# Kernel tuning notes

Hardware: AMD Instinct MI355X
Metric: run time of the kernel (lower is better)

The kernel has to match this reference:

```python
import jax, jax.numpy as jnp
import numpy as np

D_MODEL, D_INNER, D_STATE, D_CONV, DT_RANK = 192, 384, 16, 4, 12
EPS = 1e-5


def _causal_dwconv(x, w, b):
    # x: (B, L, Din); w: (Din, 1, K) depthwise; causal left pad K-1
    xc = x.transpose(0, 2, 1)  # (B, Din, L)
    y = jax.lax.conv_general_dilated(xc, w, window_strides=(1,),
                                     padding=[(D_CONV - 1, 0)],
                                     feature_group_count=D_INNER,
                                     dimension_numbers=('NCH', 'OIH', 'NCH'))
    return (y + b[None, :, None]).transpose(0, 2, 1)  # (B, L, Din)


def _ssm_dir(xh, z, conv_w, conv_b, x_proj_w, dt_w, dt_b, A_log, D):
    # one direction of the selective scan
    x = jax.nn.silu(_causal_dwconv(xh, conv_w, conv_b))  # (B, L, Din)
    x_dbl = jnp.einsum('bld,ed->ble', x, x_proj_w)       # (B, L, R+2N)
    dt = jax.nn.softplus(jnp.einsum('blr,dr->bld', x_dbl[..., :DT_RANK], dt_w) + dt_b)
    Bm = x_dbl[..., DT_RANK:DT_RANK + D_STATE]           # (B, L, N)
    Cm = x_dbl[..., DT_RANK + D_STATE:]                  # (B, L, N)
    A = -jnp.exp(A_log)                                  # (Din, N)
    deltaA = jnp.exp(dt[..., None] * A)                  # (B, L, Din, N)
    dBx = (dt * x)[..., None] * Bm[:, :, None, :]        # (B, L, Din, N)

    def comb(e1, e2):
        a1, b1 = e1
        a2, b2 = e2
        return a1 * a2, a2 * b1 + b2

    _, h = jax.lax.associative_scan(comb, (deltaA, dBx), axis=1)
    y = jnp.einsum('bldn,bln->bld', h, Cm) + x * D
    return y * jax.nn.silu(z)


def setup_inputs() -> dict:
    key = jax.random.key(0)
    ks = jax.random.split(key, 24)
    B, L = 2, 2048
    s = 0.02
    inp = {
        'hidden_states': jax.random.normal(ks[0], (B, L, D_MODEL), jnp.float32),
        'residual': jax.random.normal(ks[1], (B, L, D_MODEL), jnp.float32),
        'norm_w': jnp.ones((D_MODEL,), jnp.float32),
        'in_proj_w': jax.random.normal(ks[2], (2 * D_INNER, D_MODEL)) * s,
        'out_proj_w': jax.random.normal(ks[3], (D_MODEL, D_INNER)) * s,
        # forward-direction SSM params
        'conv_w_f': jax.random.normal(ks[4], (D_INNER, 1, D_CONV)) * s,
        'conv_b_f': jnp.zeros((D_INNER,), jnp.float32),
        'x_proj_w_f': jax.random.normal(ks[5], (DT_RANK + 2 * D_STATE, D_INNER)) * s,
        'dt_w_f': jax.random.normal(ks[6], (D_INNER, DT_RANK)) * s,
        'dt_b_f': jax.random.uniform(ks[7], (D_INNER,), minval=-4.0, maxval=-2.0),
        'A_log_f': jnp.log(jnp.tile(jnp.arange(1, D_STATE + 1, dtype=jnp.float32), (D_INNER, 1))),
        'D_f': jnp.ones((D_INNER,), jnp.float32),
        # backward-direction SSM params (bimamba)
        'conv_w_b': jax.random.normal(ks[8], (D_INNER, 1, D_CONV)) * s,
        'conv_b_b': jnp.zeros((D_INNER,), jnp.float32),
        'x_proj_w_b': jax.random.normal(ks[9], (DT_RANK + 2 * D_STATE, D_INNER)) * s,
        'dt_w_b': jax.random.normal(ks[10], (D_INNER, DT_RANK)) * s,
        'dt_b_b': jax.random.uniform(ks[11], (D_INNER,), minval=-4.0, maxval=-2.0),
        'A_log_b': jnp.log(jnp.tile(jnp.arange(1, D_STATE + 1, dtype=jnp.float32), (D_INNER, 1))),
        'D_b': jnp.ones((D_INNER,), jnp.float32),
    }
    return inp


def reference(hidden_states, residual, norm_w, in_proj_w, out_proj_w,
              conv_w_f, conv_b_f, x_proj_w_f, dt_w_f, dt_b_f, A_log_f, D_f,
              conv_w_b, conv_b_b, x_proj_w_b, dt_w_b, dt_b_b, A_log_b, D_b):
    # fused add + RMSNorm (prenorm=True): residual_out = hidden + residual (fp32)
    residual_out = (hidden_states + residual).astype(jnp.float32)
    x = residual_out * jax.lax.rsqrt(jnp.mean(residual_out * residual_out, axis=-1, keepdims=True) + EPS)
    x = x * norm_w
    # Mamba mixer, bimamba=True
    xz = jnp.einsum('bld,ed->ble', x, in_proj_w)  # (B, L, 2*Din)
    xh, z = xz[..., :D_INNER], xz[..., D_INNER:]
    y_f = _ssm_dir(xh, z, conv_w_f, conv_b_f, x_proj_w_f, dt_w_f, dt_b_f, A_log_f, D_f)
    y_b = _ssm_dir(xh[:, ::-1], z[:, ::-1], conv_w_b, conv_b_b, x_proj_w_b, dt_w_b, dt_b_b, A_log_b, D_b)[:, ::-1]
    out = jnp.einsum('bld,ed->ble', y_f + y_b, out_proj_w)
    return out, residual_out
```

## Files before the change

### kernel.cpp

```cpp
#include <hip/hip_runtime.h>
#include <math.h>

#define BB 2
#define LL 2048
#define DM 192
#define DI 384
#define DS 16
#define RK 12
#define NROW (BB*LL)
#define NCH 64
#define CLEN (LL/NCH)

typedef __attribute__((ext_vector_type(8))) short bf16x8;
typedef __attribute__((ext_vector_type(4))) float f32x4;

__device__ __forceinline__ float siluf(float v) { return v / (1.f + __expf(-v)); }

__device__ __forceinline__ unsigned short f2bf(float f) {
  unsigned int x = __float_as_uint(f);
  unsigned int r = (x + 0x7fffu + ((x >> 16) & 1u)) >> 16;
  return (unsigned short)r;
}
__device__ __forceinline__ float bf2f(unsigned short u) {
  return __uint_as_float(((unsigned int)u) << 16);
}

#define N_BFIN  (6*48*512)
#define N_BFOUT (12*12*512)
#define N_BFXP  (2*12*4*512)
#define N_DT    (2*RK*DI)
#define N_PREP  (N_BFIN + N_BFOUT + N_BFXP + N_DT)

__global__ __launch_bounds__(256) void k_wprep(
    const float* __restrict__ wip, const float* __restrict__ wop,
    const float* __restrict__ xpwf, const float* __restrict__ xpwb,
    const float* __restrict__ dtwf, const float* __restrict__ dtwb,
    unsigned short* __restrict__ bin, unsigned short* __restrict__ bout,
    unsigned short* __restrict__ bxp, float* __restrict__ wdt) {
  int i = blockIdx.x * 256 + threadIdx.x;
  if (i < N_BFIN) {
    int j = i & 7, l = (i >> 3) & 63, ng = (i >> 9) % 48, ks = i / (48 * 512);
    int k = ks * 32 + (l >> 4) * 8 + j, c = ng * 16 + (l & 15);
    bin[i] = f2bf(wip[c * DM + k]);
  } else if (i < N_BFIN + N_BFOUT) {
    int t = i - N_BFIN;
    int j = t & 7, l = (t >> 3) & 63, ng = (t >> 9) % 12, ks = t / (12 * 512);
    int k = ks * 32 + (l >> 4) * 8 + j, c = ng * 16 + (l & 15);
    bout[t] = f2bf(wop[c * DI + k]);
  } else if (i < N_BFIN + N_BFOUT + N_BFXP) {
    int t = i - N_BFIN - N_BFOUT;
    int j = t & 7, l = (t >> 3) & 63, ng = (t >> 9) & 3, ks = (t >> 11) % 12;
    int dir = t / (12 * 4 * 512);
    int k = ks * 32 + (l >> 4) * 8 + j, e = ng * 16 + (l & 15);
    const float* src = dir ? xpwb : xpwf;
    bxp[t] = (e < RK + 2 * DS) ? f2bf(src[e * DI + k]) : (unsigned short)0;
  } else if (i < N_PREP) {
    int t = i - N_BFIN - N_BFOUT - N_BFXP;
    int dir = t / (RK * DI), rem = t % (RK * DI);
    int j = rem / DI, d = rem % DI;
    const float* src = dir ? dtwb : dtwf;
    wdt[t] = src[d * RK + j];
  }
}

__global__ __launch_bounds__(256) void k_rmsnorm(
    const float* __restrict__ h, const float* __restrict__ r,
    const float* __restrict__ w, float* __restrict__ res,
    unsigned short* __restrict__ xnb) {
  int row = blockIdx.x * 4 + (threadIdx.x >> 6);
  int lane = threadIdx.x & 63;
  const float* hp = h + row * DM;
  const float* rp = r + row * DM;
  float v0 = hp[lane]       + rp[lane];
  float v1 = hp[lane + 64]  + rp[lane + 64];
  float v2 = hp[lane + 128] + rp[lane + 128];
  float ss = v0 * v0 + v1 * v1 + v2 * v2;
  #pragma unroll
  for (int o = 32; o; o >>= 1) ss += __shfl_xor(ss, o);
  float inv = rsqrtf(ss * (1.f / DM) + 1e-5f);
  float* rr = res + row * DM;
  unsigned short* xo = xnb + row * DM;
  rr[lane] = v0; rr[lane + 64] = v1; rr[lane + 128] = v2;
  xo[lane]       = f2bf(v0 * inv * w[lane]);
  xo[lane + 64]  = f2bf(v1 * inv * w[lane + 64]);
  xo[lane + 128] = f2bf(v2 * inv * w[lane + 128]);
}

__global__ __launch_bounds__(64) void k_inproj(
    const unsigned short* __restrict__ xnb, const unsigned short* __restrict__ bin,
    unsigned short* __restrict__ xhb, unsigned short* __restrict__ zb) {
  int l = threadIdx.x;
  int row0 = blockIdx.x * 16;
  int ng0 = blockIdx.y * 4;
  const unsigned short* arow = xnb + (size_t)(row0 + (l & 15)) * DM + ((l >> 4) * 8);
  f32x4 acc[4];
  #pragma unroll
  for (int g = 0; g < 4; g++) acc[g] = (f32x4){0.f, 0.f, 0.f, 0.f};
  #pragma unroll
  for (int ks = 0; ks < 6; ks++) {
    bf16x8 a = *reinterpret_cast<const bf16x8*>(arow + ks * 32);
    #pragma unroll
    for (int g = 0; g < 4; g++) {
      bf16x8 b = *reinterpret_cast<const bf16x8*>(bin + ((size_t)(ks * 48 + ng0 + g) * 64 + l) * 8);
      acc[g] = __builtin_amdgcn_mfma_f32_16x16x32_bf16(a, b, acc[g], 0, 0, 0);
    }
  }
  int rbase = row0 + (l >> 4) * 4;
  #pragma unroll
  for (int g = 0; g < 4; g++) {
    int col = (ng0 + g) * 16 + (l & 15);
    unsigned short* dst = (col < DI) ? (xhb + col) : (zb + (col - DI));
    #pragma unroll
    for (int r = 0; r < 4; r++) dst[(size_t)(rbase + r) * DI] = f2bf(acc[g][r]);
  }
}

__global__ __launch_bounds__(256) void k_conv(
    const unsigned short* __restrict__ xhb,
    const float* __restrict__ cwf, const float* __restrict__ cbf,
    const float* __restrict__ cwb, const float* __restrict__ cbb,
    unsigned short* __restrict__ xcb) {
  int dir = blockIdx.y;
  int g = blockIdx.x * 256 + threadIdx.x;
  int row = g / DI, d = g % DI;
  int b = row >> 11, s = row & (LL - 1);
  const float* cw = dir ? cwb : cwf;
  const float* cb = dir ? cbb : cbf;
  float acc = cb[d];
  #pragma unroll
  for (int k = 0; k < 4; k++) {
    int sp = s - 3 + k;
    if (sp >= 0) {
      int mr = b * LL + (dir ? (LL - 1 - sp) : sp);
      acc += cw[d * 4 + k] * bf2f(xhb[(size_t)mr * DI + d]);
    }
  }
  xcb[(size_t)(dir * NROW + row) * DI + d] = f2bf(siluf(acc));
}

__global__ __launch_bounds__(128) void k_xpmm(
    const unsigned short* __restrict__ xcb, const unsigned short* __restrict__ bxp,
    const float* __restrict__ wdt_all,
    const float* __restrict__ dtbf, const float* __restrict__ dtbb,
    float* __restrict__ dt, float* __restrict__ Bm, float* __restrict__ Cm) {
  __shared__ float xd[16][48];
  int l = threadIdx.x & 63, w = threadIdx.x >> 6;
  int dir = blockIdx.y;
  int row0 = blockIdx.x * 16;
  const unsigned short* arow = xcb + (size_t)(dir * NROW + row0 + (l & 15)) * DI + ((l >> 4) * 8);
  const unsigned short* wb = bxp + (size_t)dir * 12 * 4 * 512;
  f32x4 acc[2];
  acc[0] = (f32x4){0.f, 0.f, 0.f, 0.f};
  acc[1] = (f32x4){0.f, 0.f, 0.f, 0.f};
  #pragma unroll
  for (int ks = 0; ks < 12; ks++) {
    bf16x8 a = *reinterpret_cast<const bf16x8*>(arow + ks * 32);
    #pragma unroll
    for (int g = 0; g < 2; g++) {
      int ng = w * 2 + g;
      bf16x8 b = *reinterpret_cast<const bf16x8*>(wb + ((size_t)(ks * 4 + ng) * 64 + l) * 8);
      acc[g] = __builtin_amdgcn_mfma_f32_16x16x32_bf16(a, b, acc[g], 0, 0, 0);
    }
  }
  int rbase = (l >> 4) * 4;
  #pragma unroll
  for (int g = 0; g < 2; g++) {
    int col = (w * 2 + g) * 16 + (l & 15);
    #pragma unroll
    for (int r = 0; r < 4; r++) xd[rbase + r][col] = acc[g][r];
  }
  __syncthreads();
  const float* wdt = wdt_all + dir * RK * DI;
  const float* dtb = dir ? dtbb : dtbf;
  int t = threadIdx.x;
  #pragma unroll
  for (int i = 0; i < 48; i++) {
    int idx = i * 128 + t;
    int row = idx / DI, d = idx % DI;
    float a = dtb[d];
    #pragma unroll
    for (int j = 0; j < RK; j++) a = __fmaf_rn(xd[row][j], wdt[j * DI + d], a);
    a = (a > 20.f) ? a : log1pf(__expf(a));
    dt[(size_t)(dir * NROW + row0 + row) * DI + d] = a;
  }
  #pragma unroll
  for (int i = 0; i < 4; i++) {
    int idx = i * 128 + t;
    int row = idx / 32, j = idx % 32;
    float v = xd[row][RK + j];
    if (j < DS) Bm[(size_t)(dir * NROW + row0 + row) * DS + j] = v;
    else        Cm[(size_t)(dir * NROW + row0 + row) * DS + (j - DS)] = v;
  }
}

__global__ __launch_bounds__(128) void k_scan1(
    const float* __restrict__ dt, const unsigned short* __restrict__ xcb,
    const float* __restrict__ Bm,
    const float* __restrict__ Alf, const float* __restrict__ Alb,
    float* __restrict__ S, float* __restrict__ P) {
  int zb = blockIdx.z;
  int dir = zb >> 1;
  int d = blockIdx.x * 128 + threadIdx.x;
  int c = blockIdx.y;
  const float* Al = dir ? Alb : Alf;
  float Av[DS];
  {
    const float4* ap = reinterpret_cast<const float4*>(Al + d * DS);
    #pragma unroll
    for (int q = 0; q < 4; q++) {
      float4 a = ap[q];
      Av[4*q+0] = -__expf(a.x); Av[4*q+1] = -__expf(a.y);
      Av[4*q+2] = -__expf(a.z); Av[4*q+3] = -__expf(a.w);
    }
  }
  int rowbase = zb * LL + c * CLEN;
  const float4* Bp4 = reinterpret_cast<const float4*>(Bm + (size_t)rowbase * DS);
  float h[DS];
  #pragma unroll
  for (int n = 0; n < DS; n++) h[n] = 0.f;
  float sdt = 0.f;
  float dtv = dt[(size_t)rowbase * DI + d];
  float xv  = bf2f(xcb[(size_t)rowbase * DI + d]);
  #pragma unroll 4
  for (int s = 0; s < CLEN; s++) {
    float dtn_ = 0.f, xn_ = 0.f;
    if (s + 1 < CLEN) {
      dtn_ = dt[(size_t)(rowbase + s + 1) * DI + d];
      xn_  = bf2f(xcb[(size_t)(rowbase + s + 1) * DI + d]);
    }
    float4 B0 = Bp4[s*4+0], B1 = Bp4[s*4+1], B2 = Bp4[s*4+2], B3 = Bp4[s*4+3];
    float Bv[DS] = {B0.x,B0.y,B0.z,B0.w, B1.x,B1.y,B1.z,B1.w,
                    B2.x,B2.y,B2.z,B2.w, B3.x,B3.y,B3.z,B3.w};
    float dtx = dtv * xv;
    sdt += dtv;
    #pragma unroll
    for (int n = 0; n < DS; n++) {
      float dA = __expf(dtv * Av[n]);
      h[n] = __fmaf_rn(dA, h[n], dtx * Bv[n]);
    }
    dtv = dtn_; xv = xn_;
  }
  size_t base = ((size_t)(zb * NCH + c) * DI + d) * DS;
  float4* Sp = reinterpret_cast<float4*>(S + base);
  float4* Pp = reinterpret_cast<float4*>(P + base);
  #pragma unroll
  for (int q = 0; q < 4; q++) {
    Sp[q] = make_float4(h[4*q+0], h[4*q+1], h[4*q+2], h[4*q+3]);
    Pp[q] = make_float4(__expf(Av[4*q+0]*sdt), __expf(Av[4*q+1]*sdt),
                        __expf(Av[4*q+2]*sdt), __expf(Av[4*q+3]*sdt));
  }
}

__global__ __launch_bounds__(256) void k_scan2(
    float* __restrict__ S, const float* __restrict__ P) {
  int g = blockIdx.x * 256 + threadIdx.x;
  int zb = g / (DI * DS);
  int rem = g % (DI * DS);
  const int stride = DI * DS;
  size_t base = (size_t)zb * NCH * stride + rem;
  float carry = 0.f;
  for (int c0 = 0; c0 < NCH; c0 += 8) {
    float p8[8], s8[8];
    #pragma unroll
    for (int j = 0; j < 8; j++) {
      p8[j] = P[base + (size_t)(c0 + j) * stride];
      s8[j] = S[base + (size_t)(c0 + j) * stride];
    }
    #pragma unroll
    for (int j = 0; j < 8; j++) {
      S[base + (size_t)(c0 + j) * stride] = carry;
      carry = __fmaf_rn(p8[j], carry, s8[j]);
    }
  }
}

__global__ __launch_bounds__(128) void k_scan3(
    const float* __restrict__ dt, const unsigned short* __restrict__ xcb,
    const float* __restrict__ Bm, const float* __restrict__ Cm,
    const unsigned short* __restrict__ zb_, const float* __restrict__ Hin,
    const float* __restrict__ Alf, const float* __restrict__ Alb,
    const float* __restrict__ Df, const float* __restrict__ Db,
    unsigned short* __restrict__ yb) {
  int zbi = blockIdx.z;
  int dir = zbi >> 1, b = zbi & 1;
  int d = blockIdx.x * 128 + threadIdx.x;
  int c = blockIdx.y;
  const float* Al = dir ? Alb : Alf;
  const float* Dp = dir ? Db : Df;
  float Av[DS];
  {
    const float4* ap = reinterpret_cast<const float4*>(Al + d * DS);
    #pragma unroll
    for (int q = 0; q < 4; q++) {
      float4 a = ap[q];
      Av[4*q+0] = -__expf(a.x); Av[4*q+1] = -__expf(a.y);
      Av[4*q+2] = -__expf(a.z); Av[4*q+3] = -__expf(a.w);
    }
  }
  float Dv = Dp[d];
  int rowbase = zbi * LL + c * CLEN;
  const float4* Bp4 = reinterpret_cast<const float4*>(Bm + (size_t)rowbase * DS);
  const float4* Cp4 = reinterpret_cast<const float4*>(Cm + (size_t)rowbase * DS);
  size_t base = ((size_t)(zbi * NCH + c) * DI + d) * DS;
  float h[DS];
  {
    const float4* hp = reinterpret_cast<const float4*>(Hin + base);
    #pragma unroll
    for (int q = 0; q < 4; q++) {
      float4 a = hp[q];
      h[4*q+0] = a.x; h[4*q+1] = a.y; h[4*q+2] = a.z; h[4*q+3] = a.w;
    }
  }
  float dtv = dt[(size_t)rowbase * DI + d];
  float xv  = bf2f(xcb[(size_t)rowbase * DI + d]);
  #pragma unroll 4
  for (int s = 0; s < CLEN; s++) {
    float dtn_ = 0.f, xn_ = 0.f;
    if (s + 1 < CLEN) {
      dtn_ = dt[(size_t)(rowbase + s + 1) * DI + d];
      xn_  = bf2f(xcb[(size_t)(rowbase + s + 1) * DI + d]);
    }
    float4 B0 = Bp4[s*4+0], B1 = Bp4[s*4+1], B2 = Bp4[s*4+2], B3 = Bp4[s*4+3];
    float Bv[DS] = {B0.x,B0.y,B0.z,B0.w, B1.x,B1.y,B1.z,B1.w,
                    B2.x,B2.y,B2.z,B2.w, B3.x,B3.y,B3.z,B3.w};
    float4 C0 = Cp4[s*4+0], C1 = Cp4[s*4+1], C2 = Cp4[s*4+2], C3 = Cp4[s*4+3];
    float Cv[DS] = {C0.x,C0.y,C0.z,C0.w, C1.x,C1.y,C1.z,C1.w,
                    C2.x,C2.y,C2.z,C2.w, C3.x,C3.y,C3.z,C3.w};
    float dtx = dtv * xv;
    float acc = xv * Dv;
    #pragma unroll
    for (int n = 0; n < DS; n++) {
      float dA = __expf(dtv * Av[n]);
      h[n] = __fmaf_rn(dA, h[n], dtx * Bv[n]);
      acc = __fmaf_rn(h[n], Cv[n], acc);
    }
    int sg = c * CLEN + s;
    int mr = b * LL + (dir ? (LL - 1 - sg) : sg);
    float zv = bf2f(zb_[(size_t)mr * DI + d]);
    yb[(size_t)(rowbase + s) * DI + d] = f2bf(acc * siluf(zv));
    dtv = dtn_; xv = xn_;
  }
}

__global__ __launch_bounds__(64) void k_outproj(
    const unsigned short* __restrict__ yb, const unsigned short* __restrict__ bout,
    float* __restrict__ out) {
  int l = threadIdx.x;
  int row0 = blockIdx.x * 16;
  int ng0 = blockIdx.y * 2;
  int row = row0 + (l & 15);
  int b = row >> 11, ll = row & (LL - 1);
  const unsigned short* yf = yb + (size_t)(b * LL + ll) * DI + (l >> 4) * 8;
  const unsigned short* yr = yb + (size_t)((2 + b) * LL + (LL - 1 - ll)) * DI + (l >> 4) * 8;
  f32x4 acc[2];
  acc[0] = (f32x4){0.f, 0.f, 0.f, 0.f};
  acc[1] = (f32x4){0.f, 0.f, 0.f, 0.f};
  #pragma unroll
  for (int ks = 0; ks < 12; ks++) {
    bf16x8 f8 = *reinterpret_cast<const bf16x8*>(yf + ks * 32);
    bf16x8 g8 = *reinterpret_cast<const bf16x8*>(yr + ks * 32);
    bf16x8 a;
    #pragma unroll
    for (int j = 0; j < 8; j++)
      a[j] = (short)f2bf(bf2f((unsigned short)f8[j]) + bf2f((unsigned short)g8[j]));
    #pragma unroll
    for (int g = 0; g < 2; g++) {
      bf16x8 bb = *reinterpret_cast<const bf16x8*>(bout + ((size_t)(ks * 12 + ng0 + g) * 64 + l) * 8);
      acc[g] = __builtin_amdgcn_mfma_f32_16x16x32_bf16(a, bb, acc[g], 0, 0, 0);
    }
  }
  int rbase = row0 + (l >> 4) * 4;
  #pragma unroll
  for (int g = 0; g < 2; g++) {
    int col = (ng0 + g) * 16 + (l & 15);
    #pragma unroll
    for (int r = 0; r < 4; r++) out[(size_t)(rbase + r) * DM + col] = acc[g][r];
  }
}

extern "C" void kernel_launch(void* const* d_in, const int* in_sizes, int n_in,
                              void* d_out, int out_size, void* d_ws, size_t ws_size,
                              hipStream_t stream) {
  const float* hid  = (const float*)d_in[0];
  const float* res  = (const float*)d_in[1];
  const float* nw   = (const float*)d_in[2];
  const float* wip  = (const float*)d_in[3];
  const float* wop  = (const float*)d_in[4];
  const float* cwf  = (const float*)d_in[5];
  const float* cbf  = (const float*)d_in[6];
  const float* xpwf = (const float*)d_in[7];
  const float* dtwf = (const float*)d_in[8];
  const float* dtbf = (const float*)d_in[9];
  const float* Alf  = (const float*)d_in[10];
  const float* Df   = (const float*)d_in[11];
  const float* cwb  = (const float*)d_in[12];
  const float* cbb  = (const float*)d_in[13];
  const float* xpwb = (const float*)d_in[14];
  const float* dtwb = (const float*)d_in[15];
  const float* dtbb = (const float*)d_in[16];
  const float* Alb  = (const float*)d_in[17];
  const float* Db   = (const float*)d_in[18];

  float* out_p  = (float*)d_out;
  float* resid  = out_p + NROW * DM;

  float* ws = (float*)d_ws;
  float* dt   = ws;
  float* Bm   = dt   + 2 * NROW * DI;
  float* Cm   = Bm   + 2 * NROW * DS;
  float* S    = Cm   + 2 * NROW * DS;
  float* P    = S    + 2 * BB * NCH * DI * DS;
  float* wdt  = P    + 2 * BB * NCH * DI * DS;
  unsigned short* xnb = (unsigned short*)(wdt + N_DT);
  unsigned short* xhb = xnb + NROW * DM;
  unsigned short* zb  = xhb + NROW * DI;
  unsigned short* xcb = zb  + NROW * DI;
  unsigned short* yb  = xcb + 2 * NROW * DI;
  unsigned short* bin = yb  + 2 * NROW * DI;
  unsigned short* bout = bin + N_BFIN;
  unsigned short* bxp  = bout + N_BFOUT;

  k_wprep<<<(N_PREP + 255) / 256, 256, 0, stream>>>(wip, wop, xpwf, xpwb, dtwf, dtwb,
                                                    bin, bout, bxp, wdt);
  k_rmsnorm<<<NROW / 4, 256, 0, stream>>>(hid, res, nw, resid, xnb);
  k_inproj<<<dim3(NROW / 16, 12), 64, 0, stream>>>(xnb, bin, xhb, zb);
  k_conv<<<dim3(NROW * DI / 256, 2), 256, 0, stream>>>(xhb, cwf, cbf, cwb, cbb, xcb);
  k_xpmm<<<dim3(NROW / 16, 2), 128, 0, stream>>>(xcb, bxp, wdt, dtbf, dtbb, dt, Bm, Cm);
  k_scan1<<<dim3(DI / 128, NCH, 2 * BB), 128, 0, stream>>>(dt, xcb, Bm, Alf, Alb, S, P);
  k_scan2<<<(2 * BB * DI * DS) / 256, 256, 0, stream>>>(S, P);
  k_scan3<<<dim3(DI / 128, NCH, 2 * BB), 128, 0, stream>>>(dt, xcb, Bm, Cm, zb, S,
                                                           Alf, Alb, Df, Db, yb);
  k_outproj<<<dim3(NROW / 16, 6), 64, 0, stream>>>(yb, bout, out_p);
}
```

Measured before the change: 212.3 us.

## Store dt and conv output channel-major for vectorized scan loads; merge prep and rmsnorm

The conv kernel now tiles 32 timesteps per block and, in addition to the row-major output, writes a transposed channel-major copy through shared memory. The x-projection kernel writes dt in the same channel-major layout. The scan kernels can then read dt and x for several timesteps at once with vector loads from a contiguous per-channel stream, instead of doing strided scalar loads each step. The weight-prep and RMSNorm kernels are merged into one launch to save a launch. The cost is an extra transposed buffer and its writes, plus conv blocks that are now larger and hold a shared-memory tile.

```diff
diff --git a/kernel.cpp b/kernel.cpp
--- a/kernel.cpp
+++ b/kernel.cpp
@@ -10,6 +10,7 @@
 #define NROW (BB*LL)
 #define NCH 64
 #define CLEN (LL/NCH)
+#define CSTILE 32
 
 typedef __attribute__((ext_vector_type(8))) short bf16x8;
 typedef __attribute__((ext_vector_type(4))) float f32x4;
@@ -30,60 +31,62 @@
 #define N_BFXP  (2*12*4*512)
 #define N_DT    (2*RK*DI)
 #define N_PREP  (N_BFIN + N_BFOUT + N_BFXP + N_DT)
-
-__global__ __launch_bounds__(256) void k_wprep(
+#define PREP_BLKS 1092
+
+__global__ __launch_bounds__(256) void k_prep(
     const float* __restrict__ wip, const float* __restrict__ wop,
     const float* __restrict__ xpwf, const float* __restrict__ xpwb,
     const float* __restrict__ dtwf, const float* __restrict__ dtwb,
     unsigned short* __restrict__ bin, unsigned short* __restrict__ bout,
-    unsigned short* __restrict__ bxp, float* __restrict__ wdt) {
-  int i = blockIdx.x * 256 + threadIdx.x;
-  if (i < N_BFIN) {
-    int j = i & 7, l = (i >> 3) & 63, ng = (i >> 9) % 48, ks = i / (48 * 512);
-    int k = ks * 32 + (l >> 4) * 8 + j, c = ng * 16 + (l & 15);
-    bin[i] = f2bf(wip[c * DM + k]);
-  } else if (i < N_BFIN + N_BFOUT) {
-    int t = i - N_BFIN;
-    int j = t & 7, l = (t >> 3) & 63, ng = (t >> 9) % 12, ks = t / (12 * 512);
-    int k = ks * 32 + (l >> 4) * 8 + j, c = ng * 16 + (l & 15);
-    bout[t] = f2bf(wop[c * DI + k]);
-  } else if (i < N_BFIN + N_BFOUT + N_BFXP) {
-    int t = i - N_BFIN - N_BFOUT;
-    int j = t & 7, l = (t >> 3) & 63, ng = (t >> 9) & 3, ks = (t >> 11) % 12;
-    int dir = t / (12 * 4 * 512);
-    int k = ks * 32 + (l >> 4) * 8 + j, e = ng * 16 + (l & 15);
-    const float* src = dir ? xpwb : xpwf;
-    bxp[t] = (e < RK + 2 * DS) ? f2bf(src[e * DI + k]) : (unsigned short)0;
-  } else if (i < N_PREP) {
-    int t = i - N_BFIN - N_BFOUT - N_BFXP;
-    int dir = t / (RK * DI), rem = t % (RK * DI);
-    int j = rem / DI, d = rem % DI;
-    const float* src = dir ? dtwb : dtwf;
-    wdt[t] = src[d * RK + j];
-  }
-}
-
-__global__ __launch_bounds__(256) void k_rmsnorm(
+    unsigned short* __restrict__ bxp, float* __restrict__ wdt,
     const float* __restrict__ h, const float* __restrict__ r,
     const float* __restrict__ w, float* __restrict__ res,
     unsigned short* __restrict__ xnb) {
-  int row = blockIdx.x * 4 + (threadIdx.x >> 6);
-  int lane = threadIdx.x & 63;
-  const float* hp = h + row * DM;
-  const float* rp = r + row * DM;
-  float v0 = hp[lane]       + rp[lane];
-  float v1 = hp[lane + 64]  + rp[lane + 64];
-  float v2 = hp[lane + 128] + rp[lane + 128];
-  float ss = v0 * v0 + v1 * v1 + v2 * v2;
-  #pragma unroll
-  for (int o = 32; o; o >>= 1) ss += __shfl_xor(ss, o);
-  float inv = rsqrtf(ss * (1.f / DM) + 1e-5f);
-  float* rr = res + row * DM;
-  unsigned short* xo = xnb + row * DM;
-  rr[lane] = v0; rr[lane + 64] = v1; rr[lane + 128] = v2;
-  xo[lane]       = f2bf(v0 * inv * w[lane]);
-  xo[lane + 64]  = f2bf(v1 * inv * w[lane + 64]);
-  xo[lane + 128] = f2bf(v2 * inv * w[lane + 128]);
+  int blk = blockIdx.x;
+  if (blk < PREP_BLKS) {
+    int i = blk * 256 + threadIdx.x;
+    if (i < N_BFIN) {
+      int j = i & 7, l = (i >> 3) & 63, ng = (i >> 9) % 48, ks = i / (48 * 512);
+      int k = ks * 32 + (l >> 4) * 8 + j, c = ng * 16 + (l & 15);
+      bin[i] = f2bf(wip[c * DM + k]);
+    } else if (i < N_BFIN + N_BFOUT) {
+      int t = i - N_BFIN;
+      int j = t & 7, l = (t >> 3) & 63, ng = (t >> 9) % 12, ks = t / (12 * 512);
+      int k = ks * 32 + (l >> 4) * 8 + j, c = ng * 16 + (l & 15);
+      bout[t] = f2bf(wop[c * DI + k]);
+    } else if (i < N_BFIN + N_BFOUT + N_BFXP) {
+      int t = i - N_BFIN - N_BFOUT;
+      int j = t & 7, l = (t >> 3) & 63, ng = (t >> 9) & 3, ks = (t >> 11) % 12;
+      int dir = t / (12 * 4 * 512);
+      int k = ks * 32 + (l >> 4) * 8 + j, e = ng * 16 + (l & 15);
+      const float* src = dir ? xpwb : xpwf;
+      bxp[t] = (e < RK + 2 * DS) ? f2bf(src[e * DI + k]) : (unsigned short)0;
+    } else if (i < N_PREP) {
+      int t = i - N_BFIN - N_BFOUT - N_BFXP;
+      int dir = t / (RK * DI), rem = t % (RK * DI);
+      int j = rem / DI, d = rem % DI;
+      const float* src = dir ? dtwb : dtwf;
+      wdt[t] = src[d * RK + j];
+    }
+  } else {
+    int row = (blk - PREP_BLKS) * 4 + (threadIdx.x >> 6);
+    int lane = threadIdx.x & 63;
+    const float* hp = h + row * DM;
+    const float* rp = r + row * DM;
+    float v0 = hp[lane]       + rp[lane];
+    float v1 = hp[lane + 64]  + rp[lane + 64];
+    float v2 = hp[lane + 128] + rp[lane + 128];
+    float ss = v0 * v0 + v1 * v1 + v2 * v2;
+    #pragma unroll
+    for (int o = 32; o; o >>= 1) ss += __shfl_xor(ss, o);
+    float inv = rsqrtf(ss * (1.f / DM) + 1e-5f);
+    float* rr = res + row * DM;
+    unsigned short* xo = xnb + row * DM;
+    rr[lane] = v0; rr[lane + 64] = v1; rr[lane + 128] = v2;
+    xo[lane]       = f2bf(v0 * inv * w[lane]);
+    xo[lane + 64]  = f2bf(v1 * inv * w[lane + 64]);
+    xo[lane + 128] = f2bf(v2 * inv * w[lane + 128]);
+  }
 }
 
 __global__ __launch_bounds__(64) void k_inproj(
@@ -119,30 +122,43 @@
     const unsigned short* __restrict__ xhb,
     const float* __restrict__ cwf, const float* __restrict__ cbf,
     const float* __restrict__ cwb, const float* __restrict__ cbb,
-    unsigned short* __restrict__ xcb) {
-  int dir = blockIdx.y;
-  int g = blockIdx.x * 256 + threadIdx.x;
-  int row = g / DI, d = g % DI;
-  int b = row >> 11, s = row & (LL - 1);
+    unsigned short* __restrict__ xcb, unsigned short* __restrict__ xcT) {
+  __shared__ unsigned short tile[DI][CSTILE + 4];
+  int zbi = blockIdx.y;
+  int dir = zbi >> 1, b = zbi & 1;
+  int s0 = blockIdx.x * CSTILE;
   const float* cw = dir ? cwb : cwf;
   const float* cb = dir ? cbb : cbf;
-  float acc = cb[d];
-  #pragma unroll
-  for (int k = 0; k < 4; k++) {
-    int sp = s - 3 + k;
-    if (sp >= 0) {
-      int mr = b * LL + (dir ? (LL - 1 - sp) : sp);
-      acc += cw[d * 4 + k] * bf2f(xhb[(size_t)mr * DI + d]);
-    }
-  }
-  xcb[(size_t)(dir * NROW + row) * DI + d] = f2bf(siluf(acc));
+  for (int o = threadIdx.x; o < DI * CSTILE; o += 256) {
+    int d = o % DI;
+    int s = o / DI;
+    int sg = s0 + s;
+    float acc = cb[d];
+    #pragma unroll
+    for (int k = 0; k < 4; k++) {
+      int sp = sg - 3 + k;
+      if (sp >= 0) {
+        int mr = b * LL + (dir ? (LL - 1 - sp) : sp);
+        acc += cw[d * 4 + k] * bf2f(xhb[(size_t)mr * DI + d]);
+      }
+    }
+    unsigned short v = f2bf(siluf(acc));
+    xcb[(size_t)(zbi * LL + sg) * DI + d] = v;
+    tile[d][s] = v;
+  }
+  __syncthreads();
+  for (int o = threadIdx.x; o < DI * (CSTILE / 4); o += 256) {
+    int q = o & 7, d = o >> 3;
+    ushort4 v = *reinterpret_cast<const ushort4*>(&tile[d][q * 4]);
+    *reinterpret_cast<ushort4*>(xcT + ((size_t)(zbi * DI) + d) * LL + s0 + q * 4) = v;
+  }
 }
 
 __global__ __launch_bounds__(128) void k_xpmm(
     const unsigned short* __restrict__ xcb, const unsigned short* __restrict__ bxp,
     const float* __restrict__ wdt_all,
     const float* __restrict__ dtbf, const float* __restrict__ dtbb,
-    float* __restrict__ dt, float* __restrict__ Bm, float* __restrict__ Cm) {
+    float* __restrict__ dtT, float* __restrict__ Bm, float* __restrict__ Cm) {
   __shared__ float xd[16][48];
   int l = threadIdx.x & 63, w = threadIdx.x >> 6;
   int dir = blockIdx.y;
@@ -173,15 +189,25 @@
   const float* wdt = wdt_all + dir * RK * DI;
   const float* dtb = dir ? dtbb : dtbf;
   int t = threadIdx.x;
-  #pragma unroll
-  for (int i = 0; i < 48; i++) {
-    int idx = i * 128 + t;
-    int row = idx / DI, d = idx % DI;
-    float a = dtb[d];
-    #pragma unroll
-    for (int j = 0; j < RK; j++) a = __fmaf_rn(xd[row][j], wdt[j * DI + d], a);
-    a = (a > 20.f) ? a : log1pf(__expf(a));
-    dt[(size_t)(dir * NROW + row0 + row) * DI + d] = a;
+  int b = row0 >> 11, sloc = row0 & (LL - 1);
+  int zbi = dir * 2 + b;
+  #pragma unroll
+  for (int dd = 0; dd < 3; dd++) {
+    int d = dd * 128 + t;
+    float bias = dtb[d];
+    float a[16];
+    #pragma unroll
+    for (int r = 0; r < 16; r++) {
+      float acc2 = bias;
+      #pragma unroll
+      for (int j = 0; j < RK; j++) acc2 = __fmaf_rn(xd[r][j], wdt[j * DI + d], acc2);
+      a[r] = (acc2 > 20.f) ? acc2 : log1pf(__expf(acc2));
+    }
+    float* dst = dtT + ((size_t)(zbi * DI) + d) * LL + sloc;
+    #pragma unroll
+    for (int q = 0; q < 4; q++)
+      *reinterpret_cast<float4*>(dst + q * 4) =
+          make_float4(a[q*4], a[q*4+1], a[q*4+2], a[q*4+3]);
   }
   #pragma unroll
   for (int i = 0; i < 4; i++) {
@@ -194,7 +220,7 @@
 }
 
 __global__ __launch_bounds__(128) void k_scan1(
-    const float* __restrict__ dt, const unsigned short* __restrict__ xcb,
+    const float* __restrict__ dtT, const unsigned short* __restrict__ xcT,
     const float* __restrict__ Bm,
     const float* __restrict__ Alf, const float* __restrict__ Alb,
     float* __restrict__ S, float* __restrict__ P) {
@@ -213,32 +239,35 @@
       Av[4*q+2] = -__expf(a.z); Av[4*q+3] = -__expf(a.w);
     }
   }
+  const float4* dt4 = reinterpret_cast<const float4*>(dtT + ((size_t)(zb * DI) + d) * LL + c * CLEN);
+  const ushort4* xc4 = reinterpret_cast<const ushort4*>(xcT + ((size_t)(zb * DI) + d) * LL + c * CLEN);
   int rowbase = zb * LL + c * CLEN;
   const float4* Bp4 = reinterpret_cast<const float4*>(Bm + (size_t)rowbase * DS);
   float h[DS];
   #pragma unroll
   for (int n = 0; n < DS; n++) h[n] = 0.f;
   float sdt = 0.f;
-  float dtv = dt[(size_t)rowbase * DI + d];
-  float xv  = bf2f(xcb[(size_t)rowbase * DI + d]);
-  #pragma unroll 4
-  for (int s = 0; s < CLEN; s++) {
-    float dtn_ = 0.f, xn_ = 0.f;
-    if (s + 1 < CLEN) {
-      dtn_ = dt[(size_t)(rowbase + s + 1) * DI + d];
-      xn_  = bf2f(xcb[(size_t)(rowbase + s + 1) * DI + d]);
-    }
-    float4 B0 = Bp4[s*4+0], B1 = Bp4[s*4+1], B2 = Bp4[s*4+2], B3 = Bp4[s*4+3];
-    float Bv[DS] = {B0.x,B0.y,B0.z,B0.w, B1.x,B1.y,B1.z,B1.w,
-                    B2.x,B2.y,B2.z,B2.w, B3.x,B3.y,B3.z,B3.w};
-    float dtx = dtv * xv;
-    sdt += dtv;
-    #pragma unroll
-    for (int n = 0; n < DS; n++) {
-      float dA = __expf(dtv * Av[n]);
-      h[n] = __fmaf_rn(dA, h[n], dtx * Bv[n]);
-    }
-    dtv = dtn_; xv = xn_;
+  #pragma unroll 2
+  for (int s4 = 0; s4 < CLEN / 4; s4++) {
+    float4 dq = dt4[s4];
+    ushort4 xq = xc4[s4];
+    float dts[4] = {dq.x, dq.y, dq.z, dq.w};
+    float xs[4]  = {bf2f(xq.x), bf2f(xq.y), bf2f(xq.z), bf2f(xq.w)};
+    #pragma unroll
+    for (int k = 0; k < 4; k++) {
+      int s = s4 * 4 + k;
+      float4 B0 = Bp4[s*4+0], B1 = Bp4[s*4+1], B2 = Bp4[s*4+2], B3 = Bp4[s*4+3];
+      float Bv[DS] = {B0.x,B0.y,B0.z,B0.w, B1.x,B1.y,B1.z,B1.w,
+                      B2.x,B2.y,B2.z,B2.w, B3.x,B3.y,B3.z,B3.w};
+      float dtv = dts[k];
+      float dtx = dtv * xs[k];
+      sdt += dtv;
+      #pragma unroll
+      for (int n = 0; n < DS; n++) {
+        float dA = __expf(dtv * Av[n]);
+        h[n] = __fmaf_rn(dA, h[n], dtx * Bv[n]);
+      }
+    }
   }
   size_t base = ((size_t)(zb * NCH + c) * DI + d) * DS;
   float4* Sp = reinterpret_cast<float4*>(S + base);
@@ -275,7 +304,7 @@
 }
 
 __global__ __launch_bounds__(128) void k_scan3(
-    const float* __restrict__ dt, const unsigned short* __restrict__ xcb,
+    const float* __restrict__ dtT, const unsigned short* __restrict__ xcT,
     const float* __restrict__ Bm, const float* __restrict__ Cm,
     const unsigned short* __restrict__ zb_, const float* __restrict__ Hin,
     const float* __restrict__ Alf, const float* __restrict__ Alb,
@@ -298,6 +327,8 @@
     }
   }
   float Dv = Dp[d];
+  const float4* dt4 = reinterpret_cast<const float4*>(dtT + ((size_t)(zbi * DI) + d) * LL + c * CLEN);
+  const ushort4* xc4 = reinterpret_cast<const ushort4*>(xcT + ((size_t)(zbi * DI) + d) * LL + c * CLEN);
   int rowbase = zbi * LL + c * CLEN;
   const float4* Bp4 = reinterpret_cast<const float4*>(Bm + (size_t)rowbase * DS);
   const float4* Cp4 = reinterpret_cast<const float4*>(Cm + (size_t)rowbase * DS);
@@ -311,34 +342,36 @@
       h[4*q+0] = a.x; h[4*q+1] = a.y; h[4*q+2] = a.z; h[4*q+3] = a.w;
     }
   }
-  float dtv = dt[(size_t)rowbase * DI + d];
-  float xv  = bf2f(xcb[(size_t)rowbase * DI + d]);
-  #pragma unroll 4
-  for (int s = 0; s < CLEN; s++) {
-    float dtn_ = 0.f, xn_ = 0.f;
-    if (s + 1 < CLEN) {
-      dtn_ = dt[(size_t)(rowbase + s + 1) * DI + d];
-      xn_  = bf2f(xcb[(size_t)(rowbase + s + 1) * DI + d]);
-    }
-    float4 B0 = Bp4[s*4+0], B1 = Bp4[s*4+1], B2 = Bp4[s*4+2], B3 = Bp4[s*4+3];
-    float Bv[DS] = {B0.x,B0.y,B0.z,B0.w, B1.x,B1.y,B1.z,B1.w,
-                    B2.x,B2.y,B2.z,B2.w, B3.x,B3.y,B3.z,B3.w};
-    float4 C0 = Cp4[s*4+0], C1 = Cp4[s*4+1], C2 = Cp4[s*4+2], C3 = Cp4[s*4+3];
-    float Cv[DS] = {C0.x,C0.y,C0.z,C0.w, C1.x,C1.y,C1.z,C1.w,
-                    C2.x,C2.y,C2.z,C2.w, C3.x,C3.y,C3.z,C3.w};
-    float dtx = dtv * xv;
-    float acc = xv * Dv;
-    #pragma unroll
-    for (int n = 0; n < DS; n++) {
-      float dA = __expf(dtv * Av[n]);
-      h[n] = __fmaf_rn(dA, h[n], dtx * Bv[n]);
-      acc = __fmaf_rn(h[n], Cv[n], acc);
-    }
-    int sg = c * CLEN + s;
-    int mr = b * LL + (dir ? (LL - 1 - sg) : sg);
-    float zv = bf2f(zb_[(size_t)mr * DI + d]);
-    yb[(size_t)(rowbase + s) * DI + d] = f2bf(acc * siluf(zv));
-    dtv = dtn_; xv = xn_;
+  #pragma unroll 2
+  for (int s4 = 0; s4 < CLEN / 4; s4++) {
+    float4 dq = dt4[s4];
+    ushort4 xq = xc4[s4];
+    float dts[4] = {dq.x, dq.y, dq.z, dq.w};
+    float xs[4]  = {bf2f(xq.x), bf2f(xq.y), bf2f(xq.z), bf2f(xq.w)};
+    #pragma unroll
+    for (int k = 0; k < 4; k++) {
+      int s = s4 * 4 + k;
+      float4 B0 = Bp4[s*4+0], B1 = Bp4[s*4+1], B2 = Bp4[s*4+2], B3 = Bp4[s*4+3];
+      float Bv[DS] = {B0.x,B0.y,B0.z,B0.w, B1.x,B1.y,B1.z,B1.w,
+                      B2.x,B2.y,B2.z,B2.w, B3.x,B3.y,B3.z,B3.w};
+      float4 C0 = Cp4[s*4+0], C1 = Cp4[s*4+1], C2 = Cp4[s*4+2], C3 = Cp4[s*4+3];
+      float Cv[DS] = {C0.x,C0.y,C0.z,C0.w, C1.x,C1.y,C1.z,C1.w,
+                      C2.x,C2.y,C2.z,C2.w, C3.x,C3.y,C3.z,C3.w};
+      float dtv = dts[k];
+      float xv = xs[k];
+      float dtx = dtv * xv;
+      float acc = xv * Dv;
+      #pragma unroll
+      for (int n = 0; n < DS; n++) {
+        float dA = __expf(dtv * Av[n]);
+        h[n] = __fmaf_rn(dA, h[n], dtx * Bv[n]);
+        acc = __fmaf_rn(h[n], Cv[n], acc);
+      }
+      int sg = c * CLEN + s;
+      int mr = b * LL + (dir ? (LL - 1 - sg) : sg);
+      float zv = bf2f(zb_[(size_t)mr * DI + d]);
+      yb[(size_t)(rowbase + s) * DI + d] = f2bf(acc * siluf(zv));
+    }
   }
 }
 
@@ -405,8 +438,8 @@
   float* resid  = out_p + NROW * DM;
 
   float* ws = (float*)d_ws;
-  float* dt   = ws;
-  float* Bm   = dt   + 2 * NROW * DI;
+  float* dtT  = ws;
+  float* Bm   = dtT  + 2 * NROW * DI;
   float* Cm   = Bm   + 2 * NROW * DS;
   float* S    = Cm   + 2 * NROW * DS;
   float* P    = S    + 2 * BB * NCH * DI * DS;
@@ -415,20 +448,21 @@
   unsigned short* xhb = xnb + NROW * DM;
   unsigned short* zb  = xhb + NROW * DI;
   unsigned short* xcb = zb  + NROW * DI;
-  unsigned short* yb  = xcb + 2 * NROW * DI;
+  unsigned short* xcT = xcb + 2 * NROW * DI;
+  unsigned short* yb  = xcT + 2 * NROW * DI;
   unsigned short* bin = yb  + 2 * NROW * DI;
   unsigned short* bout = bin + N_BFIN;
   unsigned short* bxp  = bout + N_BFOUT;
 
-  k_wprep<<<(N_PREP + 255) / 256, 256, 0, stream>>>(wip, wop, xpwf, xpwb, dtwf, dtwb,
-                                                    bin, bout, bxp, wdt);
-  k_rmsnorm<<<NROW / 4, 256, 0, stream>>>(hid, res, nw, resid, xnb);
+  k_prep<<<PREP_BLKS + NROW / 4, 256, 0, stream>>>(wip, wop, xpwf, xpwb, dtwf, dtwb,
+                                                   bin, bout, bxp, wdt,
+                                                   hid, res, nw, resid, xnb);
   k_inproj<<<dim3(NROW / 16, 12), 64, 0, stream>>>(xnb, bin, xhb, zb);
-  k_conv<<<dim3(NROW * DI / 256, 2), 256, 0, stream>>>(xhb, cwf, cbf, cwb, cbb, xcb);
-  k_xpmm<<<dim3(NROW / 16, 2), 128, 0, stream>>>(xcb, bxp, wdt, dtbf, dtbb, dt, Bm, Cm);
-  k_scan1<<<dim3(DI / 128, NCH, 2 * BB), 128, 0, stream>>>(dt, xcb, Bm, Alf, Alb, S, P);
+  k_conv<<<dim3(LL / CSTILE, 2 * BB), 256, 0, stream>>>(xhb, cwf, cbf, cwb, cbb, xcb, xcT);
+  k_xpmm<<<dim3(NROW / 16, 2), 128, 0, stream>>>(xcb, bxp, wdt, dtbf, dtbb, dtT, Bm, Cm);
+  k_scan1<<<dim3(DI / 128, NCH, 2 * BB), 128, 0, stream>>>(dtT, xcT, Bm, Alf, Alb, S, P);
   k_scan2<<<(2 * BB * DI * DS) / 256, 256, 0, stream>>>(S, P);
-  k_scan3<<<dim3(DI / 128, NCH, 2 * BB), 128, 0, stream>>>(dt, xcb, Bm, Cm, zb, S,
+  k_scan3<<<dim3(DI / 128, NCH, 2 * BB), 128, 0, stream>>>(dtT, xcT, Bm, Cm, zb, S,
                                                            Alf, Alb, Df, Db, yb);
   k_outproj<<<dim3(NROW / 16, 6), 64, 0, stream>>>(yb, bout, out_p);
 }
```

New measurement: 253.8 us. 1.2x slower.
